# Kernel tuning notes

Hardware: AMD Instinct MI355X
Metric: run time of the kernel (lower is better)

## Reference

```python
import jax, jax.numpy as jnp
import numpy as np

B, L, HID = 4, 512, 512
H, DH = 8, 64  # num_attention_heads, attention_head_size (== rel embed size)


def setup_inputs() -> dict:
    key = jax.random.key(0)
    ks = jax.random.split(key, 9)
    s = 1.0 / np.sqrt(HID)
    return {
        "hidden_states": jax.random.normal(ks[0], (B, L, HID), jnp.float32),
        "heads": jnp.zeros((B, 1, L, L), jnp.float32),  # additive mask, 0 = valid arc
        "rels": jax.random.normal(ks[1], (B, L, L, DH), jnp.float32),
        "Wq": jax.random.normal(ks[2], (HID, HID), jnp.float32) * s,
        "bq": jnp.zeros((HID,), jnp.float32),
        "Wk": jax.random.normal(ks[3], (HID, HID), jnp.float32) * s,
        "bk": jnp.zeros((HID,), jnp.float32),
        "Wv": jax.random.normal(ks[4], (HID, HID), jnp.float32) * s,
        "bv": jnp.zeros((HID,), jnp.float32),
    }


def _heads_split(x):
    # (B, L, H*DH) -> (B, H, L, DH)
    return x.reshape(B, L, H, DH).transpose(0, 2, 1, 3)


def reference(hidden_states, heads, rels, Wq, bq, Wk, bk, Wv, bv):
    q = _heads_split(hidden_states @ Wq.T + bq)  # (B,H,L,DH)
    k = _heads_split(hidden_states @ Wk.T + bk)
    v = _heads_split(hidden_states @ Wv.T + bv)

    scores = jnp.einsum("bhqd,bhkd->bhqk", q, k)
    # relation-augmented scores: sum_d q[b,h,q,d] * rels[b,q,k,d]
    rel_scores = jnp.einsum("bhqd,bqkd->bhqk", q, rels)
    scores = (scores + rel_scores) / np.sqrt(DH) + heads  # heads broadcasts over H

    probs = jax.nn.softmax(scores, axis=-1)  # dropout is identity at eval

    ctx = jnp.einsum("bhqk,bhkd->bhqd", probs, v)
    # relation-weighted values: sum_k probs[b,h,q,k] * rels[b,q,k,d]
    ctx = ctx + jnp.einsum("bhqk,bqkd->bhqd", probs, rels)

    return ctx.transpose(0, 2, 1, 3).reshape(B, L, H * DH)
```

## Files before the change

### kernel.cpp

```cpp
#include <hip/hip_runtime.h>
#include <stdint.h>


__global__ __launch_bounds__(256)
void wtrans(const float* __restrict__ Wq, const float* __restrict__ Wk,
            const float* __restrict__ Wv, float* __restrict__ WT)
{
    __shared__ float tile[64*65];
    const int z  = blockIdx.z;
    const float* W = (z==0) ? Wq : (z==1) ? Wk : Wv;
    const int kt = blockIdx.x * 64;
    const int ot = blockIdx.y * 64;
    const int t  = threadIdx.x;

    {
        const int c4 = (t & 15) * 4;
        #pragma unroll
        for (int i = 0; i < 4; i++) {
            const int r = (t >> 4) + i*16;
            const float4 v4 = *(const float4*)(W + (size_t)(ot + r)*512 + kt + c4);
            tile[r*65 + c4 + 0] = v4.x;
            tile[r*65 + c4 + 1] = v4.y;
            tile[r*65 + c4 + 2] = v4.z;
            tile[r*65 + c4 + 3] = v4.w;
        }
    }
    __syncthreads();

    {
        const int c4 = (t & 15) * 4;
        float* dst = WT + (size_t)z*262144;
        #pragma unroll
        for (int i = 0; i < 4; i++) {
            const int r2 = (t >> 4) + i*16;
            float4 v4;
            v4.x = tile[(c4+0)*65 + r2];
            v4.y = tile[(c4+1)*65 + r2];
            v4.z = tile[(c4+2)*65 + r2];
            v4.w = tile[(c4+3)*65 + r2];
            *(float4*)(dst + (size_t)(kt + r2)*512 + ot + c4) = v4;
        }
    }
}

__global__ __launch_bounds__(512)
void qkv_gemm(const float* __restrict__ X, const float* __restrict__ WT,
              const float* __restrict__ bq, const float* __restrict__ bk,
              const float* __restrict__ bv,
              float* __restrict__ qf, float* __restrict__ kTb, float* __restrict__ vf)
{
    __shared__ __align__(16) float Xs[8][512];
    const int z  = blockIdx.y;
    const int m0 = blockIdx.x * 8;
    const float* WTz = WT + (size_t)z*262144;
    const float* bb  = (z==0) ? bq : (z==1) ? bk : bv;

    const int t = threadIdx.x;
    {
        const int r = t >> 6, c = (t & 63) * 8;
        const float4* src = (const float4*)(X + (size_t)(m0 + r)*512 + c);
        float4 a = src[0], b4 = src[1];
        *(float4*)(&Xs[r][c])     = a;
        *(float4*)(&Xs[r][c + 4]) = b4;
    }
    __syncthreads();

    const int o = t;
    float acc[8] = {0.f,0.f,0.f,0.f,0.f,0.f,0.f,0.f};

    #pragma unroll 4
    for (int k = 0; k < 512; k += 4) {
        const float w0 = WTz[(size_t)(k+0)*512 + o];
        const float w1 = WTz[(size_t)(k+1)*512 + o];
        const float w2 = WTz[(size_t)(k+2)*512 + o];
        const float w3 = WTz[(size_t)(k+3)*512 + o];
        #pragma unroll
        for (int m = 0; m < 8; m++) {
            const float4 x4 = *(const float4*)(&Xs[m][k]);
            acc[m] = fmaf(x4.x, w0, acc[m]);
            acc[m] = fmaf(x4.y, w1, acc[m]);
            acc[m] = fmaf(x4.z, w2, acc[m]);
            acc[m] = fmaf(x4.w, w3, acc[m]);
        }
    }

    const float bo = bb[o];
    const int b = m0 >> 9, l0 = m0 & 511;
    const int h = o >> 6,  d = o & 63;
    if (z == 1) {
        float* dst = kTb + ((size_t)(b*8 + h)*64 + d)*512 + l0;
        *(float4*)(dst + 0) = make_float4(acc[0]+bo, acc[1]+bo, acc[2]+bo, acc[3]+bo);
        *(float4*)(dst + 4) = make_float4(acc[4]+bo, acc[5]+bo, acc[6]+bo, acc[7]+bo);
    } else {
        float* dst = (z==0) ? qf : vf;
        #pragma unroll
        for (int m = 0; m < 8; m++)
            dst[((size_t)(b*8 + h)*512 + l0 + m)*64 + d] = acc[m] + bo;
    }
}

__global__ __launch_bounds__(512)
void attn_f32(const float* __restrict__ qf, const float* __restrict__ kT,
              const float* __restrict__ vf, const float* __restrict__ rels,
              const float* __restrict__ heads, float* __restrict__ out)
{
    __shared__ float S[8*512];
    __shared__ __align__(16) float qs[8*64];
    __shared__ float rl[64*65];

    const int bq = blockIdx.x;
    const int b = bq >> 9, q = bq & 511;
    const int t = threadIdx.x;
    const int h = t >> 6, lane = t & 63;

    qs[t] = qf[((size_t)(b*8 + h)*512 + q)*64 + lane];

    const float* relrow = rels  + ((size_t)(b*512 + q)*512)*64;
    const float* hrow   = heads + ((size_t)b*512 + q)*512;
    const float* kTh    = kT + ((size_t)(b*8 + h)*64)*512;

    for (int kt = 0; kt < 8; kt++) {
        __syncthreads();
        {
            const int r = t >> 3, c0 = (t & 7) * 8;
            const float4* src = (const float4*)(relrow + (size_t)(kt*64 + r)*64 + c0);
            const float4 A = src[0], B4 = src[1];
            float* w = rl + r*65 + c0;
            w[0]=A.x;  w[1]=A.y;  w[2]=A.z;  w[3]=A.w;
            w[4]=B4.x; w[5]=B4.y; w[6]=B4.z; w[7]=B4.w;
        }
        __syncthreads();

        const int k = kt*64 + lane;
        const float* rrow = rl + lane*65;
        float aq0=0.f, aq1=0.f, ar0=0.f, ar1=0.f;
        #pragma unroll 4
        for (int d = 0; d < 64; d += 4) {
            const float4 q4 = *(const float4*)(qs + h*64 + d);
            const float k0 = kTh[(size_t)(d+0)*512 + k];
            const float k1 = kTh[(size_t)(d+1)*512 + k];
            const float k2 = kTh[(size_t)(d+2)*512 + k];
            const float k3 = kTh[(size_t)(d+3)*512 + k];
            aq0 = fmaf(q4.x, k0, aq0);
            aq1 = fmaf(q4.y, k1, aq1);
            aq0 = fmaf(q4.z, k2, aq0);
            aq1 = fmaf(q4.w, k3, aq1);
            ar0 = fmaf(q4.x, rrow[d+0], ar0);
            ar1 = fmaf(q4.y, rrow[d+1], ar1);
            ar0 = fmaf(q4.z, rrow[d+2], ar0);
            ar1 = fmaf(q4.w, rrow[d+3], ar1);
        }
        S[h*512 + k] = ((aq0+aq1) + (ar0+ar1))*0.125f + hrow[k];
    }

    float mx = -3.0e38f;
    #pragma unroll
    for (int i = 0; i < 8; i++) mx = fmaxf(mx, S[h*512 + lane + 64*i]);
    #pragma unroll
    for (int w = 1; w < 64; w <<= 1) mx = fmaxf(mx, __shfl_xor(mx, w));
    float sum = 0.f;
    #pragma unroll
    for (int i = 0; i < 8; i++) {
        const float e = __expf(S[h*512 + lane + 64*i] - mx);
        S[h*512 + lane + 64*i] = e;
        sum += e;
    }
    #pragma unroll
    for (int w = 1; w < 64; w <<= 1) sum += __shfl_xor(sum, w);
    const float inv = 1.f / sum;

    float c0=0.f, c1=0.f, c2=0.f, c3=0.f;
    for (int kt = 0; kt < 8; kt++) {
        __syncthreads();
        {
            const int r = t >> 3, cc = (t & 7) * 8;
            const float4* src = (const float4*)(relrow + (size_t)(kt*64 + r)*64 + cc);
            const float4 A = src[0], B4 = src[1];
            float* w = rl + r*65 + cc;
            w[0]=A.x;  w[1]=A.y;  w[2]=A.z;  w[3]=A.w;
            w[4]=B4.x; w[5]=B4.y; w[6]=B4.z; w[7]=B4.w;
        }
        __syncthreads();

        const float* vb = vf + ((size_t)(b*8 + h)*512 + kt*64)*64 + lane;
        const float* Ph = S + h*512 + kt*64;
        #pragma unroll 4
        for (int kk = 0; kk < 64; kk += 4) {
            const float4 p4 = *(const float4*)(Ph + kk);
            c0 = fmaf(p4.x, vb[(size_t)(kk+0)*64] + rl[(kk+0)*65 + lane], c0);
            c1 = fmaf(p4.y, vb[(size_t)(kk+1)*64] + rl[(kk+1)*65 + lane], c1);
            c2 = fmaf(p4.z, vb[(size_t)(kk+2)*64] + rl[(kk+2)*65 + lane], c2);
            c3 = fmaf(p4.w, vb[(size_t)(kk+3)*64] + rl[(kk+3)*65 + lane], c3);
        }
    }
    out[((size_t)b*512 + q)*512 + h*64 + lane] = ((c0+c1) + (c2+c3)) * inv;
}

extern "C" void kernel_launch(void* const* d_in, const int* in_sizes, int n_in,
                              void* d_out, int out_size, void* d_ws, size_t ws_size,
                              hipStream_t stream)
{
    (void)in_sizes; (void)n_in; (void)out_size; (void)ws_size;

    const float* hidden = (const float*)d_in[0];
    const float* heads  = (const float*)d_in[1];
    const float* rels   = (const float*)d_in[2];
    const float* Wq = (const float*)d_in[3];
    const float* bq = (const float*)d_in[4];
    const float* Wk = (const float*)d_in[5];
    const float* bk = (const float*)d_in[6];
    const float* Wv = (const float*)d_in[7];
    const float* bv = (const float*)d_in[8];
    float* outF = (float*)d_out;

    float* ws = (float*)d_ws;
    float* qf  = ws;
    float* kTb = ws + 1048576;
    float* vf  = ws + 2097152;

    float* WT = outF;

    wtrans<<<dim3(8, 8, 3), 256, 0, stream>>>(Wq, Wk, Wv, WT);
    qkv_gemm<<<dim3(256, 3), 512, 0, stream>>>(hidden, WT, bq, bk, bv, qf, kTb, vf);
    attn_f32<<<dim3(2048), 512, 0, stream>>>(qf, kTb, vf, rels, heads, outF);
}
```

Baseline: 611.8 us.

## Rewrite attention as single-pass online softmax over four queries per block

The attention kernel now handles four query rows per block with an online (flash-style) softmax. The rels tile is loaded into XOR-swizzled shared memory once per key tile instead of twice, and the K/V loads are shared across the four queries. Probabilities are broadcast with readlane instead of going through a shared-memory score buffer. The QKV GEMM is also retiled so each thread computes an 8x4 register block over 16 rows, which cuts weight reloads but uses more registers and leaves fewer blocks to fill the GPU.

```diff
diff --git a/kernel.cpp b/kernel.cpp
--- a/kernel.cpp
+++ b/kernel.cpp
@@ -26,7 +26,6 @@
         }
     }
     __syncthreads();
-
     {
         const int c4 = (t & 15) * 4;
         float* dst = WT + (size_t)z*262144;
@@ -43,157 +42,179 @@
     }
 }
 
-__global__ __launch_bounds__(512)
+__global__ __launch_bounds__(256)
 void qkv_gemm(const float* __restrict__ X, const float* __restrict__ WT,
               const float* __restrict__ bq, const float* __restrict__ bk,
               const float* __restrict__ bv,
               float* __restrict__ qf, float* __restrict__ kTb, float* __restrict__ vf)
 {
-    __shared__ __align__(16) float Xs[8][512];
+    __shared__ __align__(16) float Xs[16][512];
     const int z  = blockIdx.y;
-    const int m0 = blockIdx.x * 8;
+    const int m0 = blockIdx.x * 16;
     const float* WTz = WT + (size_t)z*262144;
     const float* bb  = (z==0) ? bq : (z==1) ? bk : bv;
 
     const int t = threadIdx.x;
     {
-        const int r = t >> 6, c = (t & 63) * 8;
-        const float4* src = (const float4*)(X + (size_t)(m0 + r)*512 + c);
-        float4 a = src[0], b4 = src[1];
-        *(float4*)(&Xs[r][c])     = a;
-        *(float4*)(&Xs[r][c + 4]) = b4;
+        const int r = t >> 4, c0 = (t & 15) * 32;
+        const float4* src = (const float4*)(X + (size_t)(m0 + r)*512 + c0);
+        float4* dstl = (float4*)(&Xs[r][c0]);
+        #pragma unroll
+        for (int i = 0; i < 8; i++) dstl[i] = src[i];
     }
     __syncthreads();
 
-    const int o = t;
-    float acc[8] = {0.f,0.f,0.f,0.f,0.f,0.f,0.f,0.f};
-
-    #pragma unroll 4
+    const int ob   = t & 127;
+    const int msub = (t >> 7) * 8;
+    float acc[8][4] = {};
+
+    #pragma unroll 2
     for (int k = 0; k < 512; k += 4) {
-        const float w0 = WTz[(size_t)(k+0)*512 + o];
-        const float w1 = WTz[(size_t)(k+1)*512 + o];
-        const float w2 = WTz[(size_t)(k+2)*512 + o];
-        const float w3 = WTz[(size_t)(k+3)*512 + o];
-        #pragma unroll
-        for (int m = 0; m < 8; m++) {
-            const float4 x4 = *(const float4*)(&Xs[m][k]);
-            acc[m] = fmaf(x4.x, w0, acc[m]);
-            acc[m] = fmaf(x4.y, w1, acc[m]);
-            acc[m] = fmaf(x4.z, w2, acc[m]);
-            acc[m] = fmaf(x4.w, w3, acc[m]);
-        }
-    }
-
-    const float bo = bb[o];
-    const int b = m0 >> 9, l0 = m0 & 511;
-    const int h = o >> 6,  d = o & 63;
-    if (z == 1) {
-        float* dst = kTb + ((size_t)(b*8 + h)*64 + d)*512 + l0;
-        *(float4*)(dst + 0) = make_float4(acc[0]+bo, acc[1]+bo, acc[2]+bo, acc[3]+bo);
-        *(float4*)(dst + 4) = make_float4(acc[4]+bo, acc[5]+bo, acc[6]+bo, acc[7]+bo);
-    } else {
-        float* dst = (z==0) ? qf : vf;
-        #pragma unroll
-        for (int m = 0; m < 8; m++)
-            dst[((size_t)(b*8 + h)*512 + l0 + m)*64 + d] = acc[m] + bo;
+        float w[4][4];
+        #pragma unroll
+        for (int kk = 0; kk < 4; kk++)
+            #pragma unroll
+            for (int j = 0; j < 4; j++)
+                w[kk][j] = WTz[(size_t)(k+kk)*512 + ob + 128*j];
+        #pragma unroll
+        for (int mm = 0; mm < 8; mm++) {
+            const float4 x4 = *(const float4*)(&Xs[msub + mm][k]);
+            #pragma unroll
+            for (int j = 0; j < 4; j++) {
+                acc[mm][j] = fmaf(x4.x, w[0][j], acc[mm][j]);
+                acc[mm][j] = fmaf(x4.y, w[1][j], acc[mm][j]);
+                acc[mm][j] = fmaf(x4.z, w[2][j], acc[mm][j]);
+                acc[mm][j] = fmaf(x4.w, w[3][j], acc[mm][j]);
+            }
+        }
+    }
+
+    const int b     = m0 >> 9;
+    const int lbase = (m0 & 511) + msub;
+    #pragma unroll
+    for (int j = 0; j < 4; j++) {
+        const int o = ob + 128*j;
+        const float bo = bb[o];
+        const int h = o >> 6, d = o & 63;
+        if (z == 1) {
+            float* dst = kTb + ((size_t)(b*8 + h)*64 + d)*512 + lbase;
+            *(float4*)(dst + 0) = make_float4(acc[0][j]+bo, acc[1][j]+bo,
+                                              acc[2][j]+bo, acc[3][j]+bo);
+            *(float4*)(dst + 4) = make_float4(acc[4][j]+bo, acc[5][j]+bo,
+                                              acc[6][j]+bo, acc[7][j]+bo);
+        } else {
+            float* dst = ((z==0) ? qf : vf) + ((size_t)(b*8 + h)*512 + lbase)*64 + d;
+            #pragma unroll
+            for (int mm = 0; mm < 8; mm++) dst[(size_t)mm*64] = acc[mm][j] + bo;
+        }
     }
 }
 
 __global__ __launch_bounds__(512)
-void attn_f32(const float* __restrict__ qf, const float* __restrict__ kT,
-              const float* __restrict__ vf, const float* __restrict__ rels,
-              const float* __restrict__ heads, float* __restrict__ out)
-{
-    __shared__ float S[8*512];
-    __shared__ __align__(16) float qs[8*64];
-    __shared__ float rl[64*65];
-
-    const int bq = blockIdx.x;
-    const int b = bq >> 9, q = bq & 511;
-    const int t = threadIdx.x;
-    const int h = t >> 6, lane = t & 63;
-
-    qs[t] = qf[((size_t)(b*8 + h)*512 + q)*64 + lane];
-
-    const float* relrow = rels  + ((size_t)(b*512 + q)*512)*64;
-    const float* hrow   = heads + ((size_t)b*512 + q)*512;
-    const float* kTh    = kT + ((size_t)(b*8 + h)*64)*512;
+void attn_flash(const float* __restrict__ qf, const float* __restrict__ kT,
+                const float* __restrict__ vf, const float* __restrict__ rels,
+                const float* __restrict__ heads, float* __restrict__ out)
+{
+    __shared__ __align__(16) float rl[4*64*64];
+
+    const int bid = blockIdx.x;
+    const int wg  = (bid & 7) * 64 + (bid >> 3);
+    const int b   = wg >> 7;
+    const int q0  = (wg & 127) * 4;
+
+    const int t = threadIdx.x, h = t >> 6, lane = t & 63;
+
+    const float* kTh = kT + ((size_t)(b*8 + h)*64)*512;
+    const float* vfh = vf + ((size_t)(b*8 + h)*512)*64;
+    const float* qh  = qf + ((size_t)(b*8 + h)*512 + q0)*64;
+
+    float ctx[4] = {0.f, 0.f, 0.f, 0.f};
+    float m[4]   = {-3.0e38f, -3.0e38f, -3.0e38f, -3.0e38f};
+    float s[4]   = {0.f, 0.f, 0.f, 0.f};
+
+    const int sqi = t >> 7;
+    const int su  = t & 127;
+    const int sk  = su >> 1;
+    const int sdh = (su & 1) * 32;
+    const int sc4 = sdh >> 2;
+    const int skx = sk & 15;
+    const float* srcq = rels + ((size_t)(b*512 + q0 + sqi))*512*64;
+    float* wb = rl + sqi*4096 + sk*64;
 
     for (int kt = 0; kt < 8; kt++) {
         __syncthreads();
         {
-            const int r = t >> 3, c0 = (t & 7) * 8;
-            const float4* src = (const float4*)(relrow + (size_t)(kt*64 + r)*64 + c0);
-            const float4 A = src[0], B4 = src[1];
-            float* w = rl + r*65 + c0;
-            w[0]=A.x;  w[1]=A.y;  w[2]=A.z;  w[3]=A.w;
-            w[4]=B4.x; w[5]=B4.y; w[6]=B4.z; w[7]=B4.w;
+            const float* src = srcq + ((size_t)(kt*64 + sk))*64 + sdh;
+            #pragma unroll
+            for (int i = 0; i < 8; i++) {
+                const float4 v4 = *(const float4*)(src + 4*i);
+                *(float4*)(wb + 4*((sc4 + i) ^ skx)) = v4;
+            }
         }
         __syncthreads();
 
-        const int k = kt*64 + lane;
-        const float* rrow = rl + lane*65;
-        float aq0=0.f, aq1=0.f, ar0=0.f, ar1=0.f;
+        const int kg = kt*64 + lane;
+        const int kx4 = lane & 15;
+        const float* rr = rl + lane*64;
+        float sc[4] = {0.f, 0.f, 0.f, 0.f};
         #pragma unroll 4
-        for (int d = 0; d < 64; d += 4) {
-            const float4 q4 = *(const float4*)(qs + h*64 + d);
-            const float k0 = kTh[(size_t)(d+0)*512 + k];
-            const float k1 = kTh[(size_t)(d+1)*512 + k];
-            const float k2 = kTh[(size_t)(d+2)*512 + k];
-            const float k3 = kTh[(size_t)(d+3)*512 + k];
-            aq0 = fmaf(q4.x, k0, aq0);
-            aq1 = fmaf(q4.y, k1, aq1);
-            aq0 = fmaf(q4.z, k2, aq0);
-            aq1 = fmaf(q4.w, k3, aq1);
-            ar0 = fmaf(q4.x, rrow[d+0], ar0);
-            ar1 = fmaf(q4.y, rrow[d+1], ar1);
-            ar0 = fmaf(q4.z, rrow[d+2], ar0);
-            ar1 = fmaf(q4.w, rrow[d+3], ar1);
-        }
-        S[h*512 + k] = ((aq0+aq1) + (ar0+ar1))*0.125f + hrow[k];
-    }
-
-    float mx = -3.0e38f;
+        for (int d0 = 0; d0 < 64; d0 += 4) {
+            const float k0 = kTh[(size_t)(d0+0)*512 + kg];
+            const float k1 = kTh[(size_t)(d0+1)*512 + kg];
+            const float k2 = kTh[(size_t)(d0+2)*512 + kg];
+            const float k3 = kTh[(size_t)(d0+3)*512 + kg];
+            #pragma unroll
+            for (int qi = 0; qi < 4; qi++) {
+                const float4 q4 = *(const float4*)(qh + (size_t)qi*64 + d0);
+                const float4 r4 = *(const float4*)(rr + qi*4096
+                                                   + 4*((d0 >> 2) ^ kx4));
+                float a = sc[qi];
+                a = fmaf(q4.x, k0, a);  a = fmaf(q4.x, r4.x, a);
+                a = fmaf(q4.y, k1, a);  a = fmaf(q4.y, r4.y, a);
+                a = fmaf(q4.z, k2, a);  a = fmaf(q4.z, r4.z, a);
+                a = fmaf(q4.w, k3, a);  a = fmaf(q4.w, r4.w, a);
+                sc[qi] = a;
+            }
+        }
+
+        float P[4];
+        #pragma unroll
+        for (int qi = 0; qi < 4; qi++) {
+            float S = sc[qi]*0.125f
+                    + heads[((size_t)(b*512 + q0 + qi))*512 + kg];
+            float mt = S;
+            #pragma unroll
+            for (int w = 1; w < 64; w <<= 1) mt = fmaxf(mt, __shfl_xor(mt, w));
+            const float mn = fmaxf(m[qi], mt);
+            const float al = __expf(m[qi] - mn);
+            const float p  = __expf(S - mn);
+            float ps = p;
+            #pragma unroll
+            for (int w = 1; w < 64; w <<= 1) ps += __shfl_xor(ps, w);
+            s[qi]   = s[qi]*al + ps;
+            ctx[qi] = ctx[qi]*al;
+            m[qi]   = mn;
+            P[qi]   = p;
+        }
+
+        const float* vtile = vfh + (size_t)(kt*64)*64 + lane;
+        const int l3 = lane & 3, lc = lane >> 2;
+        #pragma unroll 8
+        for (int kk = 0; kk < 64; kk++) {
+            const float v = vtile[(size_t)kk*64];
+            const float* rb = rl + kk*64 + (l3 | ((lc ^ (kk & 15)) << 2));
+            #pragma unroll
+            for (int qi = 0; qi < 4; qi++) {
+                const float pk = __int_as_float(
+                    __builtin_amdgcn_readlane(__float_as_int(P[qi]), kk));
+                ctx[qi] = fmaf(pk, v + rb[qi*4096], ctx[qi]);
+            }
+        }
+    }
+
     #pragma unroll
-    for (int i = 0; i < 8; i++) mx = fmaxf(mx, S[h*512 + lane + 64*i]);
-    #pragma unroll
-    for (int w = 1; w < 64; w <<= 1) mx = fmaxf(mx, __shfl_xor(mx, w));
-    float sum = 0.f;
-    #pragma unroll
-    for (int i = 0; i < 8; i++) {
-        const float e = __expf(S[h*512 + lane + 64*i] - mx);
-        S[h*512 + lane + 64*i] = e;
-        sum += e;
-    }
-    #pragma unroll
-    for (int w = 1; w < 64; w <<= 1) sum += __shfl_xor(sum, w);
-    const float inv = 1.f / sum;
-
-    float c0=0.f, c1=0.f, c2=0.f, c3=0.f;
-    for (int kt = 0; kt < 8; kt++) {
-        __syncthreads();
-        {
-            const int r = t >> 3, cc = (t & 7) * 8;
-            const float4* src = (const float4*)(relrow + (size_t)(kt*64 + r)*64 + cc);
-            const float4 A = src[0], B4 = src[1];
-            float* w = rl + r*65 + cc;
-            w[0]=A.x;  w[1]=A.y;  w[2]=A.z;  w[3]=A.w;
-            w[4]=B4.x; w[5]=B4.y; w[6]=B4.z; w[7]=B4.w;
-        }
-        __syncthreads();
-
-        const float* vb = vf + ((size_t)(b*8 + h)*512 + kt*64)*64 + lane;
-        const float* Ph = S + h*512 + kt*64;
-        #pragma unroll 4
-        for (int kk = 0; kk < 64; kk += 4) {
-            const float4 p4 = *(const float4*)(Ph + kk);
-            c0 = fmaf(p4.x, vb[(size_t)(kk+0)*64] + rl[(kk+0)*65 + lane], c0);
-            c1 = fmaf(p4.y, vb[(size_t)(kk+1)*64] + rl[(kk+1)*65 + lane], c1);
-            c2 = fmaf(p4.z, vb[(size_t)(kk+2)*64] + rl[(kk+2)*65 + lane], c2);
-            c3 = fmaf(p4.w, vb[(size_t)(kk+3)*64] + rl[(kk+3)*65 + lane], c3);
-        }
-    }
-    out[((size_t)b*512 + q)*512 + h*64 + lane] = ((c0+c1) + (c2+c3)) * inv;
+    for (int qi = 0; qi < 4; qi++)
+        out[((size_t)(b*512 + q0 + qi))*512 + h*64 + lane] = ctx[qi] / s[qi];
 }
 
 extern "C" void kernel_launch(void* const* d_in, const int* in_sizes, int n_in,
@@ -221,6 +242,6 @@
     float* WT = outF;
 
     wtrans<<<dim3(8, 8, 3), 256, 0, stream>>>(Wq, Wk, Wv, WT);
-    qkv_gemm<<<dim3(256, 3), 512, 0, stream>>>(hidden, WT, bq, bk, bv, qf, kTb, vf);
-    attn_f32<<<dim3(2048), 512, 0, stream>>>(qf, kTb, vf, rels, heads, outF);
-}
+    qkv_gemm<<<dim3(128, 3), 256, 0, stream>>>(hidden, WT, bq, bk, bv, qf, kTb, vf);
+    attn_flash<<<dim3(512), 512, 0, stream>>>(qf, kTb, vf, rels, heads, outF);
+}
```

New measurement: 581.1 us. 1.05x faster.
